# Performance work log

Hardware: AMD Instinct MI355X
Metric: run time of the kernel (lower is better)

Reference implementation:

```python
import jax, jax.numpy as jnp
import numpy as np

DIM = 1024
HIDDEN = 2048
NUM_EXPERTS = 8
TOP_K = 2


def setup_inputs() -> dict:
    key = jax.random.key(0)
    ks = jax.random.split(key, 6)
    scale = 0.02
    x = jax.random.normal(ks[0], (2, 4096, DIM), dtype=jnp.float32)
    # router: Linear(dim, num_experts, bias=False) -> weight [E, d]
    router_w = jax.random.normal(ks[1], (NUM_EXPERTS, DIM), dtype=jnp.float32) * scale
    # per-expert MLP: Linear(d, h) -> w1 [E, h, d], b1 [E, h]; Linear(h, d) -> w2 [E, d, h], b2 [E, d]
    w1 = jax.random.normal(ks[2], (NUM_EXPERTS, HIDDEN, DIM), dtype=jnp.float32) * scale
    b1 = jnp.zeros((NUM_EXPERTS, HIDDEN), dtype=jnp.float32)
    w2 = jax.random.normal(ks[3], (NUM_EXPERTS, DIM, HIDDEN), dtype=jnp.float32) * scale
    b2 = jnp.zeros((NUM_EXPERTS, DIM), dtype=jnp.float32)
    return {"x": x, "router_w": router_w, "w1": w1, "b1": b1, "w2": w2, "b2": b2}


def reference(x, router_w, w1, b1, w2, b2):
    b, s, d = x.shape
    xf = x.reshape(-1, d)                              # [T, d]
    logits = xf @ router_w.T                           # [T, E]
    all_probs = jax.nn.softmax(logits, axis=-1)
    topk_logits, topk_inds = jax.lax.top_k(logits, TOP_K)   # [T, K]
    topk_probs = jax.nn.softmax(topk_logits, axis=-1)
    E = router_w.shape[0]
    onehot = jax.nn.one_hot(topk_inds, E, dtype=xf.dtype)   # [T, K, E]
    # combine weights per (token, expert); zero where expert not selected
    gate = jnp.einsum('tke,tk->te', onehot, topk_probs)     # [T, E]
    # load-balancing auxiliary loss
    f_i = onehot.mean(axis=(0, 1))                          # [E]
    P_i = all_probs.mean(axis=0)                            # [E]
    aux_loss = E * jnp.sum(f_i * P_i)
    # dense per-expert MLP, weighted combine (dropout=0 / eval mode)
    out = jnp.zeros_like(xf)
    for e in range(E):  # fixed small loop over experts
        h = jax.nn.gelu(xf @ w1[e].T + b1[e], approximate=False)  # exact GELU (torch default)
        y = h @ w2[e].T + b2[e]
        out = out + gate[:, e:e + 1] * y
    return out.reshape(b, s, d), aux_loss
```

## Files before the change

kernel.cpp:

```cpp
#include <hip/hip_runtime.h>


#define TOKS 8192
#define DIMD 1024
#define HID  2048
#define NE   8

#define OFF_COUNTS   0
#define OFF_OFFSETS  64
#define OFF_CURSORS  128
#define OFF_TILEOFF  192
#define OFF_TOPKI    256
#define OFF_TOPKG    (OFF_TOPKI + TOKS*2*4)
#define OFF_BLKPS    (OFF_TOPKG + TOKS*2*4)
#define OFF_ATOK     (OFF_BLKPS + 2048*NE*4)
#define OFF_AGATE    (OFF_ATOK + TOKS*2*4)
#define OFF_PINV     (OFF_AGATE + TOKS*2*4)
#define OFF_XG       (1u << 20)
#define XG_ROWS      (TOKS*2 + 128)
#define OFF_W1B      (OFF_XG  + (size_t)XG_ROWS * DIMD * 2)
#define OFF_W2B      (OFF_W1B + (size_t)NE * HID * DIMD * 2)
#define OFF_H        (OFF_W2B + (size_t)NE * DIMD * HID * 2)
#define OFF_Y        (OFF_H   + (size_t)XG_ROWS * HID * 2)

typedef __bf16 bf16x8 __attribute__((ext_vector_type(8)));
typedef float  floatx4 __attribute__((ext_vector_type(4)));

__device__ __forceinline__ float bf2f(unsigned short u) {
    return __uint_as_float(((unsigned)u) << 16);
}
__device__ __forceinline__ unsigned short f2bf(float f) {
    unsigned u = __float_as_uint(f);
    unsigned r = (u + 0x7FFFu + ((u >> 16) & 1u)) >> 16;
    return (unsigned short)r;
}

#define GLOBAL_AS(p) ((const __attribute__((address_space(1))) unsigned int*)(p))
#define LDS_AS(p)    ((__attribute__((address_space(3))) unsigned int*)(p))

__global__ void convert_w_kernel(const float4* __restrict__ w1,
                                 ushort4* __restrict__ w1b, int n1,
                                 const float4* __restrict__ w2,
                                 ushort4* __restrict__ w2b, int n2) {
    int i = blockIdx.x * blockDim.x + threadIdx.x;
    int stride = gridDim.x * blockDim.x;
    int ntot = n1 + n2;
    for (; i < ntot; i += stride) {
        float4 v; ushort4 o;
        if (i < n1) v = w1[i]; else v = w2[i - n1];
        o.x = f2bf(v.x); o.y = f2bf(v.y); o.z = f2bf(v.z); o.w = f2bf(v.w);
        if (i < n1) w1b[i] = o; else w2b[i - n1] = o;
    }
}

__global__ __launch_bounds__(256) void router_kernel(
    const float* __restrict__ x, const float* __restrict__ rw,
    int* __restrict__ topki, float* __restrict__ topkg,
    float* __restrict__ blkps)
{
    int wave = threadIdx.x >> 6;
    int lane = threadIdx.x & 63;
    int t = blockIdx.x * 4 + wave;
    const float* xt = x + (size_t)t * DIMD;

    float acc[NE];
#pragma unroll
    for (int e = 0; e < NE; e++) acc[e] = 0.f;
    for (int i = 0; i < DIMD / 64; i++) {
        float xv = xt[lane + 64 * i];
#pragma unroll
        for (int e = 0; e < NE; e++) acc[e] += xv * rw[e * DIMD + lane + 64 * i];
    }
#pragma unroll
    for (int off = 32; off > 0; off >>= 1) {
#pragma unroll
        for (int e = 0; e < NE; e++) acc[e] += __shfl_down(acc[e], off);
    }

    __shared__ float ps[4][NE];
    if (lane == 0) {
        float m = acc[0];
#pragma unroll
        for (int e = 1; e < NE; e++) m = fmaxf(m, acc[e]);
        float ex[NE], s = 0.f;
#pragma unroll
        for (int e = 0; e < NE; e++) { ex[e] = expf(acc[e] - m); s += ex[e]; }
        float inv = 1.f / s;
#pragma unroll
        for (int e = 0; e < NE; e++) ps[wave][e] = ex[e] * inv;

        int i0 = 0; float l0 = acc[0];
#pragma unroll
        for (int e = 1; e < NE; e++) if (acc[e] > l0) { l0 = acc[e]; i0 = e; }
        int i1 = -1; float l1 = -3.4e38f;
#pragma unroll
        for (int e = 0; e < NE; e++) if (e != i0 && acc[e] > l1) { l1 = acc[e]; i1 = e; }
        float e1 = expf(l1 - l0);
        float g0 = 1.f / (1.f + e1);
        float g1 = e1 * g0;
        topki[t * 2 + 0] = i0; topki[t * 2 + 1] = i1;
        topkg[t * 2 + 0] = g0; topkg[t * 2 + 1] = g1;
    }
    __syncthreads();
    if (threadIdx.x < NE) {
        float s = ps[0][threadIdx.x] + ps[1][threadIdx.x] + ps[2][threadIdx.x] + ps[3][threadIdx.x];
        blkps[blockIdx.x * NE + threadIdx.x] = s;
    }
}

__global__ __launch_bounds__(256) void finalize_kernel(
    const int* __restrict__ topki, const float* __restrict__ blkps,
    int* __restrict__ counts, int* __restrict__ offsets, int* __restrict__ cursors,
    int* __restrict__ tileoff, float* __restrict__ aux_out)
{
    __shared__ float psum[NE];
    __shared__ int cnt[NE];
    int tid = threadIdx.x;
    if (tid < NE) { psum[tid] = 0.f; cnt[tid] = 0; }
    __syncthreads();

    float lp[NE]; int lc[NE];
#pragma unroll
    for (int e = 0; e < NE; e++) { lp[e] = 0.f; lc[e] = 0; }
    const float4* bp4 = (const float4*)blkps;
    for (int i = tid; i < 2048 * NE / 4; i += 256) {
        float4 v = bp4[i];
        int eb = (4 * i) & 7;
        lp[eb + 0] += v.x; lp[eb + 1] += v.y; lp[eb + 2] += v.z; lp[eb + 3] += v.w;
    }
    const int4* ti4 = (const int4*)topki;
    for (int i = tid; i < TOKS * 2 / 4; i += 256) {
        int4 v = ti4[i];
        lc[v.x]++; lc[v.y]++; lc[v.z]++; lc[v.w]++;
    }
#pragma unroll
    for (int e = 0; e < NE; e++) { atomicAdd(&psum[e], lp[e]); atomicAdd(&cnt[e], lc[e]); }
    __syncthreads();

    if (tid == 0) {
        int off = 0, to = 0;
        for (int e = 0; e < NE; e++) {
            counts[e] = cnt[e];
            offsets[e] = off; cursors[e] = off;
            tileoff[e] = to;
            off += cnt[e];
            to += (cnt[e] + 127) >> 7;
        }
        offsets[NE] = off; tileoff[NE] = to;
        float aux = 0.f;
        for (int e = 0; e < NE; e++)
            aux += ((float)cnt[e] / (float)(TOKS * 2)) * (psum[e] / (float)TOKS);
        aux_out[0] = (float)NE * aux;
    }
}

__global__ __launch_bounds__(64) void fill_kernel(
    const int* __restrict__ topki, const float* __restrict__ topkg,
    int* __restrict__ cursors, int* __restrict__ atok, float* __restrict__ agate,
    int* __restrict__ posinv)
{
    int lane = threadIdx.x;
    int t = blockIdx.x * 64 + lane;
    unsigned long long below = (lane == 63) ? 0x7FFFFFFFFFFFFFFFull
                                            : ((1ull << lane) - 1ull);
#pragma unroll
    for (int k = 0; k < 2; k++) {
        int e = topki[t * 2 + k];
        float g = topkg[t * 2 + k];
        for (int ee = 0; ee < NE; ee++) {
            bool pred = (e == ee);
            unsigned long long mask = __ballot(pred ? 1 : 0);
            if (mask) {
                int leader = __ffsll((unsigned long long)mask) - 1;
                int base = 0;
                if (lane == leader) base = atomicAdd(&cursors[ee], (int)__popcll(mask));
                base = __shfl(base, leader);
                if (pred) {
                    int pos = base + (int)__popcll(mask & below);
                    atok[pos] = t;
                    agate[pos] = g;
                    posinv[t * 2 + k] = pos;
                }
            }
        }
    }
}

__global__ __launch_bounds__(256) void gather_x_kernel(
    const float* __restrict__ x, const int* __restrict__ atok,
    ushort* __restrict__ Xg)
{
    int r = blockIdx.x;
    int tid = threadIdx.x;
    int tok = atok[r];
    float4 v = ((const float4*)(x + (size_t)tok * DIMD))[tid];
    ushort4 o;
    o.x = f2bf(v.x); o.y = f2bf(v.y); o.z = f2bf(v.z); o.w = f2bf(v.w);
    ((ushort4*)(Xg + (size_t)r * DIMD))[tid] = o;
}

__global__ __launch_bounds__(256) void phase1_kernel(
    const ushort* __restrict__ Xg, const ushort* __restrict__ w1b,
    const float* __restrict__ b1,
    const int* __restrict__ counts, const int* __restrict__ offsets,
    const int* __restrict__ tileoff, unsigned short* __restrict__ Hbuf)
{
    const int NCOLT = HID / 128;
    int total = tileoff[NE] * NCOLT;
    int idx = blockIdx.x;
    if (idx >= total) return;
    int ct = idx & (NCOLT - 1);
    int rowt = idx / NCOLT;
    int e = 0;
    while (rowt >= tileoff[e + 1]) e++;
    int row0 = (rowt - tileoff[e]) * 128;
    int cnt = counts[e];
    int base = offsets[e];
    int colbase = ct * 128;

    __shared__ ushort ldsA[128 * 32];
    __shared__ ushort ldsB[128 * 32];

    int tid = threadIdx.x;
    int lane = tid & 63;
    int wave = tid >> 6;
    int wrow = wave >> 1, wcol = wave & 1;
    int l15 = lane & 15, quad = lane >> 4;

    const ushort* gA0 = Xg + (size_t)(base + row0 + 16 * (2 * wave)     + l15) * DIMD + quad * 8;
    const ushort* gA1 = Xg + (size_t)(base + row0 + 16 * (2 * wave + 1) + l15) * DIMD + quad * 8;
    const ushort* wB  = w1b + (size_t)e * HID * DIMD;
    const ushort* gB0 = wB + (size_t)(colbase + 16 * (2 * wave)     + l15) * DIMD + quad * 8;
    const ushort* gB1 = wB + (size_t)(colbase + 16 * (2 * wave + 1) + l15) * DIMD + quad * 8;

    ushort* ldA0 = &ldsA[(2 * wave) * 512];
    ushort* ldA1 = &ldsA[(2 * wave + 1) * 512];
    ushort* ldB0 = &ldsB[(2 * wave) * 512];
    ushort* ldB1 = &ldsB[(2 * wave + 1) * 512];

    floatx4 acc[4][4];
#pragma unroll
    for (int i = 0; i < 4; i++)
#pragma unroll
        for (int j = 0; j < 4; j++) acc[i][j] = (floatx4){0.f, 0.f, 0.f, 0.f};

    const bf16x8* fA = reinterpret_cast<const bf16x8*>(ldsA);
    const bf16x8* fB = reinterpret_cast<const bf16x8*>(ldsB);

    for (int k0 = 0; k0 < DIMD; k0 += 32) {
        __syncthreads();
        __builtin_amdgcn_global_load_lds(GLOBAL_AS(gA0), LDS_AS(ldA0), 16, 0, 0);
        __builtin_amdgcn_global_load_lds(GLOBAL_AS(gA1), LDS_AS(ldA1), 16, 0, 0);
        __builtin_amdgcn_global_load_lds(GLOBAL_AS(gB0), LDS_AS(ldB0), 16, 0, 0);
        __builtin_amdgcn_global_load_lds(GLOBAL_AS(gB1), LDS_AS(ldB1), 16, 0, 0);
        gA0 += 32; gA1 += 32; gB0 += 32; gB1 += 32;
        __syncthreads();

        bf16x8 a[4], b[4];
#pragma unroll
        for (int i = 0; i < 4; i++) a[i] = fA[(4 * wrow + i) * 64 + lane];
#pragma unroll
        for (int j = 0; j < 4; j++) b[j] = fB[(4 * wcol + j) * 64 + lane];
#pragma unroll
        for (int i = 0; i < 4; i++)
#pragma unroll
            for (int j = 0; j < 4; j++)
                acc[i][j] = __builtin_amdgcn_mfma_f32_16x16x32_bf16(a[i], b[j], acc[i][j], 0, 0, 0);
    }

#pragma unroll
    for (int i = 0; i < 4; i++) {
#pragma unroll
        for (int r = 0; r < 4; r++) {
            int pr = row0 + 64 * wrow + 16 * i + quad * 4 + r;
            if (pr < cnt) {
                size_t hrow = (size_t)(base + pr) * HID;
#pragma unroll
                for (int j = 0; j < 4; j++) {
                    int col = colbase + 64 * wcol + 16 * j + l15;
                    float v = acc[i][j][r] + b1[e * HID + col];
                    v = 0.5f * v * (1.f + erff(v * 0.70710678118654752f));
                    Hbuf[hrow + col] = f2bf(v);
                }
            }
        }
    }
}

__global__ __launch_bounds__(256) void phase2_kernel(
    const ushort* __restrict__ Hbuf, const ushort* __restrict__ w2b,
    const int* __restrict__ counts, const int* __restrict__ offsets,
    const int* __restrict__ tileoff, ushort* __restrict__ Y)
{
    const int NCOLT = DIMD / 128;
    int total = tileoff[NE] * NCOLT;
    int idx = blockIdx.x;
    if (idx >= total) return;
    int ct = idx & (NCOLT - 1);
    int rowt = idx / NCOLT;
    int e = 0;
    while (rowt >= tileoff[e + 1]) e++;
    int row0 = (rowt - tileoff[e]) * 128;
    int cnt = counts[e];
    int base = offsets[e];
    int colbase = ct * 128;

    __shared__ ushort ldsA[128 * 32];
    __shared__ ushort ldsB[128 * 32];

    int tid = threadIdx.x;
    int lane = tid & 63;
    int wave = tid >> 6;
    int wrow = wave >> 1, wcol = wave & 1;
    int l15 = lane & 15, quad = lane >> 4;

    const ushort* gA0 = Hbuf + (size_t)(base + row0 + 16 * (2 * wave)     + l15) * HID + quad * 8;
    const ushort* gA1 = Hbuf + (size_t)(base + row0 + 16 * (2 * wave + 1) + l15) * HID + quad * 8;
    const ushort* wB  = w2b + (size_t)e * DIMD * HID;
    const ushort* gB0 = wB + (size_t)(colbase + 16 * (2 * wave)     + l15) * HID + quad * 8;
    const ushort* gB1 = wB + (size_t)(colbase + 16 * (2 * wave + 1) + l15) * HID + quad * 8;

    ushort* ldA0 = &ldsA[(2 * wave) * 512];
    ushort* ldA1 = &ldsA[(2 * wave + 1) * 512];
    ushort* ldB0 = &ldsB[(2 * wave) * 512];
    ushort* ldB1 = &ldsB[(2 * wave + 1) * 512];

    floatx4 acc[4][4];
#pragma unroll
    for (int i = 0; i < 4; i++)
#pragma unroll
        for (int j = 0; j < 4; j++) acc[i][j] = (floatx4){0.f, 0.f, 0.f, 0.f};

    const bf16x8* fA = reinterpret_cast<const bf16x8*>(ldsA);
    const bf16x8* fB = reinterpret_cast<const bf16x8*>(ldsB);

    for (int k0 = 0; k0 < HID; k0 += 32) {
        __syncthreads();
        __builtin_amdgcn_global_load_lds(GLOBAL_AS(gA0), LDS_AS(ldA0), 16, 0, 0);
        __builtin_amdgcn_global_load_lds(GLOBAL_AS(gA1), LDS_AS(ldA1), 16, 0, 0);
        __builtin_amdgcn_global_load_lds(GLOBAL_AS(gB0), LDS_AS(ldB0), 16, 0, 0);
        __builtin_amdgcn_global_load_lds(GLOBAL_AS(gB1), LDS_AS(ldB1), 16, 0, 0);
        gA0 += 32; gA1 += 32; gB0 += 32; gB1 += 32;
        __syncthreads();

        bf16x8 a[4], b[4];
#pragma unroll
        for (int i = 0; i < 4; i++) a[i] = fA[(4 * wrow + i) * 64 + lane];
#pragma unroll
        for (int j = 0; j < 4; j++) b[j] = fB[(4 * wcol + j) * 64 + lane];
#pragma unroll
        for (int i = 0; i < 4; i++)
#pragma unroll
            for (int j = 0; j < 4; j++)
                acc[i][j] = __builtin_amdgcn_mfma_f32_16x16x32_bf16(a[i], b[j], acc[i][j], 0, 0, 0);
    }

#pragma unroll
    for (int i = 0; i < 4; i++) {
#pragma unroll
        for (int r = 0; r < 4; r++) {
            int pr = row0 + 64 * wrow + 16 * i + quad * 4 + r;
            if (pr < cnt) {
                size_t yrow = (size_t)(base + pr) * DIMD;
#pragma unroll
                for (int j = 0; j < 4; j++) {
                    int col = colbase + 64 * wcol + 16 * j + l15;
                    Y[yrow + col] = f2bf(acc[i][j][r]);
                }
            }
        }
    }
}

__global__ __launch_bounds__(256) void combine_kernel(
    const ushort* __restrict__ Y, const float* __restrict__ b2,
    const int* __restrict__ topki, const float* __restrict__ topkg,
    const int* __restrict__ posinv, float* __restrict__ out)
{
    int wave = threadIdx.x >> 6;
    int lane = threadIdx.x & 63;
    int t = blockIdx.x * 4 + wave;
    int e0 = topki[t * 2 + 0], e1 = topki[t * 2 + 1];
    float g0 = topkg[t * 2 + 0], g1 = topkg[t * 2 + 1];
    int p0 = posinv[t * 2 + 0], p1 = posinv[t * 2 + 1];

    const ushort4* y0 = (const ushort4*)(Y + (size_t)p0 * DIMD);
    const ushort4* y1 = (const ushort4*)(Y + (size_t)p1 * DIMD);
    const float4* b20 = (const float4*)(b2 + (size_t)e0 * DIMD);
    const float4* b21 = (const float4*)(b2 + (size_t)e1 * DIMD);
    float4* o4 = (float4*)(out + (size_t)t * DIMD);

#pragma unroll
    for (int c = 0; c < DIMD / 4 / 64; c++) {
        int i = lane + 64 * c;
        ushort4 a = y0[i], b = y1[i];
        float4 ba = b20[i], bb = b21[i];
        float4 r;
        r.x = g0 * (bf2f(a.x) + ba.x) + g1 * (bf2f(b.x) + bb.x);
        r.y = g0 * (bf2f(a.y) + ba.y) + g1 * (bf2f(b.y) + bb.y);
        r.z = g0 * (bf2f(a.z) + ba.z) + g1 * (bf2f(b.z) + bb.z);
        r.w = g0 * (bf2f(a.w) + ba.w) + g1 * (bf2f(b.w) + bb.w);
        o4[i] = r;
    }
}

extern "C" void kernel_launch(void* const* d_in, const int* in_sizes, int n_in,
                              void* d_out, int out_size, void* d_ws, size_t ws_size,
                              hipStream_t stream) {
    const float* x  = (const float*)d_in[0];
    const float* rw = (const float*)d_in[1];
    const float* w1 = (const float*)d_in[2];
    const float* b1 = (const float*)d_in[3];
    const float* w2 = (const float*)d_in[4];
    const float* b2 = (const float*)d_in[5];
    float* out = (float*)d_out;

    char* ws = (char*)d_ws;
    int*   counts  = (int*)(ws + OFF_COUNTS);
    int*   offsets = (int*)(ws + OFF_OFFSETS);
    int*   cursors = (int*)(ws + OFF_CURSORS);
    int*   tileoff = (int*)(ws + OFF_TILEOFF);
    int*   topki   = (int*)(ws + OFF_TOPKI);
    float* topkg   = (float*)(ws + OFF_TOPKG);
    float* blkps   = (float*)(ws + OFF_BLKPS);
    int*   atok    = (int*)(ws + OFF_ATOK);
    float* agate   = (float*)(ws + OFF_AGATE);
    int*   posinv  = (int*)(ws + OFF_PINV);
    ushort* Xg     = (ushort*)(ws + OFF_XG);
    ushort* w1b    = (ushort*)(ws + OFF_W1B);
    ushort* w2b    = (ushort*)(ws + OFF_W2B);
    ushort* Hbuf   = (ushort*)(ws + OFF_H);
    ushort* Y      = (ushort*)(ws + OFF_Y);

    convert_w_kernel<<<8192, 256, 0, stream>>>(
        (const float4*)w1, (ushort4*)w1b, NE * HID * DIMD / 4,
        (const float4*)w2, (ushort4*)w2b, NE * DIMD * HID / 4);

    router_kernel<<<TOKS / 4, 256, 0, stream>>>(x, rw, topki, topkg, blkps);
    finalize_kernel<<<1, 256, 0, stream>>>(topki, blkps, counts, offsets, cursors,
                                           tileoff, out + (size_t)TOKS * DIMD);
    fill_kernel<<<TOKS / 64, 64, 0, stream>>>(topki, topkg, cursors, atok, agate,
                                              posinv);
    gather_x_kernel<<<TOKS * 2, 256, 0, stream>>>(x, atok, Xg);

    phase1_kernel<<<135 * (HID / 128), 256, 0, stream>>>(
        Xg, w1b, b1, counts, offsets, tileoff, Hbuf);
    phase2_kernel<<<135 * (DIMD / 128), 256, 0, stream>>>(
        Hbuf, w2b, counts, offsets, tileoff, Y);
    combine_kernel<<<TOKS / 4, 256, 0, stream>>>(Y, b2, topki, topkg, posinv, out);
}
```

Measured before the change: 634.3 us.

## Double-buffer LDS tiles with K=64 steps and remap block order in expert GEMMs

Both grouped GEMM kernels now keep two LDS buffers and issue the async global-to-LDS loads for the next K=64 slab before running the MFMAs on the current slab. This lets memory loads overlap compute and halves the number of barriers per K step. Block indices are also permuted (stride of gridDim/8) so that neighbouring blocks are spread across XCDs. The cost is 4x the LDS per block (64KB), which may reduce occupancy. The remap assumes the grid size is a multiple of 8, otherwise some tiles are skipped.

```diff
diff --git a/kernel.cpp b/kernel.cpp
--- a/kernel.cpp
+++ b/kernel.cpp
@@ -207,7 +207,8 @@
 {
     const int NCOLT = HID / 128;
     int total = tileoff[NE] * NCOLT;
-    int idx = blockIdx.x;
+    int q = (int)(gridDim.x >> 3);
+    int idx = (int)(blockIdx.x & 7) * q + (int)(blockIdx.x >> 3);
     if (idx >= total) return;
     int ct = idx & (NCOLT - 1);
     int rowt = idx / NCOLT;
@@ -218,8 +219,7 @@
     int base = offsets[e];
     int colbase = ct * 128;
 
-    __shared__ ushort ldsA[128 * 32];
-    __shared__ ushort ldsB[128 * 32];
+    __shared__ ushort lds[2][2][2][128 * 32];
 
     int tid = threadIdx.x;
     int lane = tid & 63;
@@ -227,16 +227,20 @@
     int wrow = wave >> 1, wcol = wave & 1;
     int l15 = lane & 15, quad = lane >> 4;
 
-    const ushort* gA0 = Xg + (size_t)(base + row0 + 16 * (2 * wave)     + l15) * DIMD + quad * 8;
-    const ushort* gA1 = Xg + (size_t)(base + row0 + 16 * (2 * wave + 1) + l15) * DIMD + quad * 8;
-    const ushort* wB  = w1b + (size_t)e * HID * DIMD;
-    const ushort* gB0 = wB + (size_t)(colbase + 16 * (2 * wave)     + l15) * DIMD + quad * 8;
-    const ushort* gB1 = wB + (size_t)(colbase + 16 * (2 * wave + 1) + l15) * DIMD + quad * 8;
-
-    ushort* ldA0 = &ldsA[(2 * wave) * 512];
-    ushort* ldA1 = &ldsA[(2 * wave + 1) * 512];
-    ushort* ldB0 = &ldsB[(2 * wave) * 512];
-    ushort* ldB1 = &ldsB[(2 * wave + 1) * 512];
+    const ushort* gA = Xg + (size_t)(base + row0 + 16 * (2 * wave) + l15) * DIMD + quad * 8;
+    const ushort* gB = w1b + (size_t)e * HID * DIMD
+                     + (size_t)(colbase + 16 * (2 * wave) + l15) * DIMD + quad * 8;
+
+#define P1_STAGE(BUF, KOFF) do { \
+    __builtin_amdgcn_global_load_lds(GLOBAL_AS(gA + (KOFF)),                  LDS_AS(&lds[BUF][0][0][(2*wave+0)*512]), 16, 0, 0); \
+    __builtin_amdgcn_global_load_lds(GLOBAL_AS(gA + (KOFF) + 16*DIMD),        LDS_AS(&lds[BUF][0][0][(2*wave+1)*512]), 16, 0, 0); \
+    __builtin_amdgcn_global_load_lds(GLOBAL_AS(gA + (KOFF) + 32),             LDS_AS(&lds[BUF][0][1][(2*wave+0)*512]), 16, 0, 0); \
+    __builtin_amdgcn_global_load_lds(GLOBAL_AS(gA + (KOFF) + 32 + 16*DIMD),   LDS_AS(&lds[BUF][0][1][(2*wave+1)*512]), 16, 0, 0); \
+    __builtin_amdgcn_global_load_lds(GLOBAL_AS(gB + (KOFF)),                  LDS_AS(&lds[BUF][1][0][(2*wave+0)*512]), 16, 0, 0); \
+    __builtin_amdgcn_global_load_lds(GLOBAL_AS(gB + (KOFF) + 16*DIMD),        LDS_AS(&lds[BUF][1][0][(2*wave+1)*512]), 16, 0, 0); \
+    __builtin_amdgcn_global_load_lds(GLOBAL_AS(gB + (KOFF) + 32),             LDS_AS(&lds[BUF][1][1][(2*wave+0)*512]), 16, 0, 0); \
+    __builtin_amdgcn_global_load_lds(GLOBAL_AS(gB + (KOFF) + 32 + 16*DIMD),   LDS_AS(&lds[BUF][1][1][(2*wave+1)*512]), 16, 0, 0); \
+} while (0)
 
     floatx4 acc[4][4];
 #pragma unroll
@@ -244,29 +248,52 @@
 #pragma unroll
         for (int j = 0; j < 4; j++) acc[i][j] = (floatx4){0.f, 0.f, 0.f, 0.f};
 
-    const bf16x8* fA = reinterpret_cast<const bf16x8*>(ldsA);
-    const bf16x8* fB = reinterpret_cast<const bf16x8*>(ldsB);
-
-    for (int k0 = 0; k0 < DIMD; k0 += 32) {
+    P1_STAGE(0, 0);
+    __syncthreads();
+
+    int cur = 0;
+    for (int kt = 0; kt < DIMD / 64 - 1; kt++) {
+        bf16x8 a[2][4], b[2][4];
+#pragma unroll
+        for (int h = 0; h < 2; h++) {
+            const bf16x8* fA = (const bf16x8*)&lds[cur][0][h][0];
+            const bf16x8* fB = (const bf16x8*)&lds[cur][1][h][0];
+#pragma unroll
+            for (int i = 0; i < 4; i++) a[h][i] = fA[(4 * wrow + i) * 64 + lane];
+#pragma unroll
+            for (int j = 0; j < 4; j++) b[h][j] = fB[(4 * wcol + j) * 64 + lane];
+        }
+        P1_STAGE(cur ^ 1, (kt + 1) * 64);
+#pragma unroll
+        for (int h = 0; h < 2; h++)
+#pragma unroll
+            for (int i = 0; i < 4; i++)
+#pragma unroll
+                for (int j = 0; j < 4; j++)
+                    acc[i][j] = __builtin_amdgcn_mfma_f32_16x16x32_bf16(a[h][i], b[h][j], acc[i][j], 0, 0, 0);
         __syncthreads();
-        __builtin_amdgcn_global_load_lds(GLOBAL_AS(gA0), LDS_AS(ldA0), 16, 0, 0);
-        __builtin_amdgcn_global_load_lds(GLOBAL_AS(gA1), LDS_AS(ldA1), 16, 0, 0);
-        __builtin_amdgcn_global_load_lds(GLOBAL_AS(gB0), LDS_AS(ldB0), 16, 0, 0);
-        __builtin_amdgcn_global_load_lds(GLOBAL_AS(gB1), LDS_AS(ldB1), 16, 0, 0);
-        gA0 += 32; gA1 += 32; gB0 += 32; gB1 += 32;
-        __syncthreads();
-
-        bf16x8 a[4], b[4];
-#pragma unroll
-        for (int i = 0; i < 4; i++) a[i] = fA[(4 * wrow + i) * 64 + lane];
-#pragma unroll
-        for (int j = 0; j < 4; j++) b[j] = fB[(4 * wcol + j) * 64 + lane];
-#pragma unroll
-        for (int i = 0; i < 4; i++)
-#pragma unroll
-            for (int j = 0; j < 4; j++)
-                acc[i][j] = __builtin_amdgcn_mfma_f32_16x16x32_bf16(a[i], b[j], acc[i][j], 0, 0, 0);
-    }
+        cur ^= 1;
+    }
+    {
+        bf16x8 a[2][4], b[2][4];
+#pragma unroll
+        for (int h = 0; h < 2; h++) {
+            const bf16x8* fA = (const bf16x8*)&lds[cur][0][h][0];
+            const bf16x8* fB = (const bf16x8*)&lds[cur][1][h][0];
+#pragma unroll
+            for (int i = 0; i < 4; i++) a[h][i] = fA[(4 * wrow + i) * 64 + lane];
+#pragma unroll
+            for (int j = 0; j < 4; j++) b[h][j] = fB[(4 * wcol + j) * 64 + lane];
+        }
+#pragma unroll
+        for (int h = 0; h < 2; h++)
+#pragma unroll
+            for (int i = 0; i < 4; i++)
+#pragma unroll
+                for (int j = 0; j < 4; j++)
+                    acc[i][j] = __builtin_amdgcn_mfma_f32_16x16x32_bf16(a[h][i], b[h][j], acc[i][j], 0, 0, 0);
+    }
+#undef P1_STAGE
 
 #pragma unroll
     for (int i = 0; i < 4; i++) {
@@ -294,7 +321,8 @@
 {
     const int NCOLT = DIMD / 128;
     int total = tileoff[NE] * NCOLT;
-    int idx = blockIdx.x;
+    int q = (int)(gridDim.x >> 3);
+    int idx = (int)(blockIdx.x & 7) * q + (int)(blockIdx.x >> 3);
     if (idx >= total) return;
     int ct = idx & (NCOLT - 1);
     int rowt = idx / NCOLT;
@@ -305,8 +333,7 @@
     int base = offsets[e];
     int colbase = ct * 128;
 
-    __shared__ ushort ldsA[128 * 32];
-    __shared__ ushort ldsB[128 * 32];
+    __shared__ ushort lds[2][2][2][128 * 32];
 
     int tid = threadIdx.x;
     int lane = tid & 63;
@@ -314,16 +341,20 @@
     int wrow = wave >> 1, wcol = wave & 1;
     int l15 = lane & 15, quad = lane >> 4;
 
-    const ushort* gA0 = Hbuf + (size_t)(base + row0 + 16 * (2 * wave)     + l15) * HID + quad * 8;
-    const ushort* gA1 = Hbuf + (size_t)(base + row0 + 16 * (2 * wave + 1) + l15) * HID + quad * 8;
-    const ushort* wB  = w2b + (size_t)e * DIMD * HID;
-    const ushort* gB0 = wB + (size_t)(colbase + 16 * (2 * wave)     + l15) * HID + quad * 8;
-    const ushort* gB1 = wB + (size_t)(colbase + 16 * (2 * wave + 1) + l15) * HID + quad * 8;
-
-    ushort* ldA0 = &ldsA[(2 * wave) * 512];
-    ushort* ldA1 = &ldsA[(2 * wave + 1) * 512];
-    ushort* ldB0 = &ldsB[(2 * wave) * 512];
-    ushort* ldB1 = &ldsB[(2 * wave + 1) * 512];
+    const ushort* gA = Hbuf + (size_t)(base + row0 + 16 * (2 * wave) + l15) * HID + quad * 8;
+    const ushort* gB = w2b + (size_t)e * DIMD * HID
+                     + (size_t)(colbase + 16 * (2 * wave) + l15) * HID + quad * 8;
+
+#define P2_STAGE(BUF, KOFF) do { \
+    __builtin_amdgcn_global_load_lds(GLOBAL_AS(gA + (KOFF)),                 LDS_AS(&lds[BUF][0][0][(2*wave+0)*512]), 16, 0, 0); \
+    __builtin_amdgcn_global_load_lds(GLOBAL_AS(gA + (KOFF) + 16*HID),        LDS_AS(&lds[BUF][0][0][(2*wave+1)*512]), 16, 0, 0); \
+    __builtin_amdgcn_global_load_lds(GLOBAL_AS(gA + (KOFF) + 32),            LDS_AS(&lds[BUF][0][1][(2*wave+0)*512]), 16, 0, 0); \
+    __builtin_amdgcn_global_load_lds(GLOBAL_AS(gA + (KOFF) + 32 + 16*HID),   LDS_AS(&lds[BUF][0][1][(2*wave+1)*512]), 16, 0, 0); \
+    __builtin_amdgcn_global_load_lds(GLOBAL_AS(gB + (KOFF)),                 LDS_AS(&lds[BUF][1][0][(2*wave+0)*512]), 16, 0, 0); \
+    __builtin_amdgcn_global_load_lds(GLOBAL_AS(gB + (KOFF) + 16*HID),        LDS_AS(&lds[BUF][1][0][(2*wave+1)*512]), 16, 0, 0); \
+    __builtin_amdgcn_global_load_lds(GLOBAL_AS(gB + (KOFF) + 32),            LDS_AS(&lds[BUF][1][1][(2*wave+0)*512]), 16, 0, 0); \
+    __builtin_amdgcn_global_load_lds(GLOBAL_AS(gB + (KOFF) + 32 + 16*HID),   LDS_AS(&lds[BUF][1][1][(2*wave+1)*512]), 16, 0, 0); \
+} while (0)
 
     floatx4 acc[4][4];
 #pragma unroll
@@ -331,29 +362,52 @@
 #pragma unroll
         for (int j = 0; j < 4; j++) acc[i][j] = (floatx4){0.f, 0.f, 0.f, 0.f};
 
-    const bf16x8* fA = reinterpret_cast<const bf16x8*>(ldsA);
-    const bf16x8* fB = reinterpret_cast<const bf16x8*>(ldsB);
-
-    for (int k0 = 0; k0 < HID; k0 += 32) {
+    P2_STAGE(0, 0);
+    __syncthreads();
+
+    int cur = 0;
+    for (int kt = 0; kt < HID / 64 - 1; kt++) {
+        bf16x8 a[2][4], b[2][4];
+#pragma unroll
+        for (int h = 0; h < 2; h++) {
+            const bf16x8* fA = (const bf16x8*)&lds[cur][0][h][0];
+            const bf16x8* fB = (const bf16x8*)&lds[cur][1][h][0];
+#pragma unroll
+            for (int i = 0; i < 4; i++) a[h][i] = fA[(4 * wrow + i) * 64 + lane];
+#pragma unroll
+            for (int j = 0; j < 4; j++) b[h][j] = fB[(4 * wcol + j) * 64 + lane];
+        }
+        P2_STAGE(cur ^ 1, (kt + 1) * 64);
+#pragma unroll
+        for (int h = 0; h < 2; h++)
+#pragma unroll
+            for (int i = 0; i < 4; i++)
+#pragma unroll
+                for (int j = 0; j < 4; j++)
+                    acc[i][j] = __builtin_amdgcn_mfma_f32_16x16x32_bf16(a[h][i], b[h][j], acc[i][j], 0, 0, 0);
         __syncthreads();
-        __builtin_amdgcn_global_load_lds(GLOBAL_AS(gA0), LDS_AS(ldA0), 16, 0, 0);
-        __builtin_amdgcn_global_load_lds(GLOBAL_AS(gA1), LDS_AS(ldA1), 16, 0, 0);
-        __builtin_amdgcn_global_load_lds(GLOBAL_AS(gB0), LDS_AS(ldB0), 16, 0, 0);
-        __builtin_amdgcn_global_load_lds(GLOBAL_AS(gB1), LDS_AS(ldB1), 16, 0, 0);
-        gA0 += 32; gA1 += 32; gB0 += 32; gB1 += 32;
-        __syncthreads();
-
-        bf16x8 a[4], b[4];
-#pragma unroll
-        for (int i = 0; i < 4; i++) a[i] = fA[(4 * wrow + i) * 64 + lane];
-#pragma unroll
-        for (int j = 0; j < 4; j++) b[j] = fB[(4 * wcol + j) * 64 + lane];
-#pragma unroll
-        for (int i = 0; i < 4; i++)
-#pragma unroll
-            for (int j = 0; j < 4; j++)
-                acc[i][j] = __builtin_amdgcn_mfma_f32_16x16x32_bf16(a[i], b[j], acc[i][j], 0, 0, 0);
-    }
+        cur ^= 1;
+    }
+    {
+        bf16x8 a[2][4], b[2][4];
+#pragma unroll
+        for (int h = 0; h < 2; h++) {
+            const bf16x8* fA = (const bf16x8*)&lds[cur][0][h][0];
+            const bf16x8* fB = (const bf16x8*)&lds[cur][1][h][0];
+#pragma unroll
+            for (int i = 0; i < 4; i++) a[h][i] = fA[(4 * wrow + i) * 64 + lane];
+#pragma unroll
+            for (int j = 0; j < 4; j++) b[h][j] = fB[(4 * wcol + j) * 64 + lane];
+        }
+#pragma unroll
+        for (int h = 0; h < 2; h++)
+#pragma unroll
+            for (int i = 0; i < 4; i++)
+#pragma unroll
+                for (int j = 0; j < 4; j++)
+                    acc[i][j] = __builtin_amdgcn_mfma_f32_16x16x32_bf16(a[h][i], b[h][j], acc[i][j], 0, 0, 0);
+    }
+#undef P2_STAGE
 
 #pragma unroll
     for (int i = 0; i < 4; i++) {
```

New measurement: 683.3 us. +7.7%, slower.

## Enlarge grouped GEMM tiles to 256x256, double-buffer LDS, remap blocks across XCDs

Applied to the files above, without the earlier changes.

Both expert GEMM phases move from 128x128 tiles with 256 threads to 256x256 tiles with 512 threads. Each wave now accumulates an 8x4 grid of MFMA tiles. The K-step grows to 64, and LDS is double-buffered so the next global-to-LDS load is issued before computing on the current buffer, leaving one barrier per step instead of two. Block IDs are remapped so consecutive tiles land on the same XCD for L2 reuse, and the bias load is hoisted out of the store loop. In exchange there are fewer blocks, which hurts load balance, more padding rows per expert, and higher register pressure from 128 accumulator floats per thread.

```diff
diff --git a/kernel.cpp b/kernel.cpp
--- a/kernel.cpp
+++ b/kernel.cpp
@@ -17,7 +17,7 @@
 #define OFF_AGATE    (OFF_ATOK + TOKS*2*4)
 #define OFF_PINV     (OFF_AGATE + TOKS*2*4)
 #define OFF_XG       (1u << 20)
-#define XG_ROWS      (TOKS*2 + 128)
+#define XG_ROWS      (TOKS*2 + 256)
 #define OFF_W1B      (OFF_XG  + (size_t)XG_ROWS * DIMD * 2)
 #define OFF_W2B      (OFF_W1B + (size_t)NE * HID * DIMD * 2)
 #define OFF_H        (OFF_W2B + (size_t)NE * DIMD * HID * 2)
@@ -37,6 +37,13 @@
 
 #define GLOBAL_AS(p) ((const __attribute__((address_space(1))) unsigned int*)(p))
 #define LDS_AS(p)    ((__attribute__((address_space(3))) unsigned int*)(p))
+
+__device__ __forceinline__ int xcd_remap(int bid, int nwg) {
+    int xcd = bid & 7, pos = bid >> 3;
+    int q = nwg >> 3, r = nwg & 7;
+    int start = (xcd < r) ? xcd * (q + 1) : r * (q + 1) + (xcd - r) * q;
+    return start + pos;
+}
 
 __global__ void convert_w_kernel(const float4* __restrict__ w1,
                                  ushort4* __restrict__ w1b, int n1,
@@ -144,7 +151,7 @@
             offsets[e] = off; cursors[e] = off;
             tileoff[e] = to;
             off += cnt[e];
-            to += (cnt[e] + 127) >> 7;
+            to += (cnt[e] + 255) >> 8;
         }
         offsets[NE] = off; tileoff[NE] = to;
         float aux = 0.f;
@@ -199,86 +206,108 @@
     ((ushort4*)(Xg + (size_t)r * DIMD))[tid] = o;
 }
 
-__global__ __launch_bounds__(256) void phase1_kernel(
+
+__global__ __launch_bounds__(512, 2) void phase1_kernel(
     const ushort* __restrict__ Xg, const ushort* __restrict__ w1b,
     const float* __restrict__ b1,
     const int* __restrict__ counts, const int* __restrict__ offsets,
     const int* __restrict__ tileoff, unsigned short* __restrict__ Hbuf)
 {
-    const int NCOLT = HID / 128;
+    const int LD = DIMD;
+    const int NT = DIMD / 64;
+    const int NCOLT = HID / 256;
     int total = tileoff[NE] * NCOLT;
-    int idx = blockIdx.x;
+    int idx = xcd_remap((int)blockIdx.x, (int)gridDim.x);
     if (idx >= total) return;
     int ct = idx & (NCOLT - 1);
     int rowt = idx / NCOLT;
     int e = 0;
     while (rowt >= tileoff[e + 1]) e++;
-    int row0 = (rowt - tileoff[e]) * 128;
+    int row0 = (rowt - tileoff[e]) * 256;
     int cnt = counts[e];
     int base = offsets[e];
-    int colbase = ct * 128;
-
-    __shared__ ushort ldsA[128 * 32];
-    __shared__ ushort ldsB[128 * 32];
+    int colbase = ct * 256;
+
+    __shared__ ushort lds[2][64][512];
 
     int tid = threadIdx.x;
     int lane = tid & 63;
     int wave = tid >> 6;
-    int wrow = wave >> 1, wcol = wave & 1;
+    int wr = wave >> 2, wc = wave & 3;
     int l15 = lane & 15, quad = lane >> 4;
 
-    const ushort* gA0 = Xg + (size_t)(base + row0 + 16 * (2 * wave)     + l15) * DIMD + quad * 8;
-    const ushort* gA1 = Xg + (size_t)(base + row0 + 16 * (2 * wave + 1) + l15) * DIMD + quad * 8;
-    const ushort* wB  = w1b + (size_t)e * HID * DIMD;
-    const ushort* gB0 = wB + (size_t)(colbase + 16 * (2 * wave)     + l15) * DIMD + quad * 8;
-    const ushort* gB1 = wB + (size_t)(colbase + 16 * (2 * wave + 1) + l15) * DIMD + quad * 8;
-
-    ushort* ldA0 = &ldsA[(2 * wave) * 512];
-    ushort* ldA1 = &ldsA[(2 * wave + 1) * 512];
-    ushort* ldB0 = &ldsB[(2 * wave) * 512];
-    ushort* ldB1 = &ldsB[(2 * wave + 1) * 512];
-
-    floatx4 acc[4][4];
-#pragma unroll
-    for (int i = 0; i < 4; i++)
+    const ushort* gApanel = Xg + (size_t)(base + row0) * LD;
+    const ushort* gBpanel = w1b + (size_t)e * HID * DIMD + (size_t)colbase * LD;
+
+    const ushort* src[8];
+#pragma unroll
+    for (int i = 0; i < 8; i++) {
+        int chunk = wave * 8 + i;
+        int tensor = chunk >> 5;
+        int r = chunk & 31;
+        int s = r >> 1, h = r & 1;
+        const ushort* bse = tensor ? gBpanel : gApanel;
+        src[i] = bse + (size_t)(s * 16 + l15) * LD + h * 32 + quad * 8;
+    }
+
+#define STAGE(BUF) do { \
+    _Pragma("unroll") \
+    for (int i = 0; i < 8; i++) { \
+        __builtin_amdgcn_global_load_lds(GLOBAL_AS(src[i]), LDS_AS(&lds[BUF][wave*8 + i][0]), 16, 0, 0); \
+        src[i] += 64; \
+    } \
+} while (0)
+
+    floatx4 acc[8][4];
+#pragma unroll
+    for (int i = 0; i < 8; i++)
 #pragma unroll
         for (int j = 0; j < 4; j++) acc[i][j] = (floatx4){0.f, 0.f, 0.f, 0.f};
 
-    const bf16x8* fA = reinterpret_cast<const bf16x8*>(ldsA);
-    const bf16x8* fB = reinterpret_cast<const bf16x8*>(ldsB);
-
-    for (int k0 = 0; k0 < DIMD; k0 += 32) {
+    auto compute = [&](int bufidx) {
+        const bf16x8* C = (const bf16x8*)&lds[bufidx][0][0];
+#pragma unroll
+        for (int h = 0; h < 2; h++) {
+            bf16x8 a[8], b[4];
+#pragma unroll
+            for (int i = 0; i < 8; i++) a[i] = C[((wr * 8 + i) * 2 + h) * 64 + lane];
+#pragma unroll
+            for (int j = 0; j < 4; j++) b[j] = C[(32 + (wc * 4 + j) * 2 + h) * 64 + lane];
+#pragma unroll
+            for (int i = 0; i < 8; i++)
+#pragma unroll
+                for (int j = 0; j < 4; j++)
+                    acc[i][j] = __builtin_amdgcn_mfma_f32_16x16x32_bf16(a[i], b[j], acc[i][j], 0, 0, 0);
+        }
+    };
+
+    STAGE(0);
+    __syncthreads();
+    int cur = 0;
+    for (int kt = 0; kt < NT - 1; kt++) {
+        STAGE(cur ^ 1);
+        compute(cur);
         __syncthreads();
-        __builtin_amdgcn_global_load_lds(GLOBAL_AS(gA0), LDS_AS(ldA0), 16, 0, 0);
-        __builtin_amdgcn_global_load_lds(GLOBAL_AS(gA1), LDS_AS(ldA1), 16, 0, 0);
-        __builtin_amdgcn_global_load_lds(GLOBAL_AS(gB0), LDS_AS(ldB0), 16, 0, 0);
-        __builtin_amdgcn_global_load_lds(GLOBAL_AS(gB1), LDS_AS(ldB1), 16, 0, 0);
-        gA0 += 32; gA1 += 32; gB0 += 32; gB1 += 32;
-        __syncthreads();
-
-        bf16x8 a[4], b[4];
-#pragma unroll
-        for (int i = 0; i < 4; i++) a[i] = fA[(4 * wrow + i) * 64 + lane];
-#pragma unroll
-        for (int j = 0; j < 4; j++) b[j] = fB[(4 * wcol + j) * 64 + lane];
-#pragma unroll
-        for (int i = 0; i < 4; i++)
-#pragma unroll
-            for (int j = 0; j < 4; j++)
-                acc[i][j] = __builtin_amdgcn_mfma_f32_16x16x32_bf16(a[i], b[j], acc[i][j], 0, 0, 0);
-    }
-
-#pragma unroll
-    for (int i = 0; i < 4; i++) {
-#pragma unroll
-        for (int r = 0; r < 4; r++) {
-            int pr = row0 + 64 * wrow + 16 * i + quad * 4 + r;
+        cur ^= 1;
+    }
+    compute(cur);
+#undef STAGE
+
+    float b1v[4];
+#pragma unroll
+    for (int j = 0; j < 4; j++)
+        b1v[j] = b1[e * HID + colbase + 64 * wc + 16 * j + l15];
+#pragma unroll
+    for (int i = 0; i < 8; i++) {
+#pragma unroll
+        for (int rr = 0; rr < 4; rr++) {
+            int pr = row0 + 128 * wr + 16 * i + quad * 4 + rr;
             if (pr < cnt) {
                 size_t hrow = (size_t)(base + pr) * HID;
 #pragma unroll
                 for (int j = 0; j < 4; j++) {
-                    int col = colbase + 64 * wcol + 16 * j + l15;
-                    float v = acc[i][j][r] + b1[e * HID + col];
+                    int col = colbase + 64 * wc + 16 * j + l15;
+                    float v = acc[i][j][rr] + b1v[j];
                     v = 0.5f * v * (1.f + erff(v * 0.70710678118654752f));
                     Hbuf[hrow + col] = f2bf(v);
                 }
@@ -287,85 +316,102 @@
     }
 }
 
-__global__ __launch_bounds__(256) void phase2_kernel(
+__global__ __launch_bounds__(512, 2) void phase2_kernel(
     const ushort* __restrict__ Hbuf, const ushort* __restrict__ w2b,
     const int* __restrict__ counts, const int* __restrict__ offsets,
     const int* __restrict__ tileoff, ushort* __restrict__ Y)
 {
-    const int NCOLT = DIMD / 128;
+    const int LD = HID;
+    const int NT = HID / 64;
+    const int NCOLT = DIMD / 256;
     int total = tileoff[NE] * NCOLT;
-    int idx = blockIdx.x;
+    int idx = xcd_remap((int)blockIdx.x, (int)gridDim.x);
     if (idx >= total) return;
     int ct = idx & (NCOLT - 1);
     int rowt = idx / NCOLT;
     int e = 0;
     while (rowt >= tileoff[e + 1]) e++;
-    int row0 = (rowt - tileoff[e]) * 128;
+    int row0 = (rowt - tileoff[e]) * 256;
     int cnt = counts[e];
     int base = offsets[e];
-    int colbase = ct * 128;
-
-    __shared__ ushort ldsA[128 * 32];
-    __shared__ ushort ldsB[128 * 32];
+    int colbase = ct * 256;
+
+    __shared__ ushort lds[2][64][512];
 
     int tid = threadIdx.x;
     int lane = tid & 63;
     int wave = tid >> 6;
-    int wrow = wave >> 1, wcol = wave & 1;
+    int wr = wave >> 2, wc = wave & 3;
     int l15 = lane & 15, quad = lane >> 4;
 
-    const ushort* gA0 = Hbuf + (size_t)(base + row0 + 16 * (2 * wave)     + l15) * HID + quad * 8;
-    const ushort* gA1 = Hbuf + (size_t)(base + row0 + 16 * (2 * wave + 1) + l15) * HID + quad * 8;
-    const ushort* wB  = w2b + (size_t)e * DIMD * HID;
-    const ushort* gB0 = wB + (size_t)(colbase + 16 * (2 * wave)     + l15) * HID + quad * 8;
-    const ushort* gB1 = wB + (size_t)(colbase + 16 * (2 * wave + 1) + l15) * HID + quad * 8;
-
-    ushort* ldA0 = &ldsA[(2 * wave) * 512];
-    ushort* ldA1 = &ldsA[(2 * wave + 1) * 512];
-    ushort* ldB0 = &ldsB[(2 * wave) * 512];
-    ushort* ldB1 = &ldsB[(2 * wave + 1) * 512];
-
-    floatx4 acc[4][4];
-#pragma unroll
-    for (int i = 0; i < 4; i++)
+    const ushort* gApanel = Hbuf + (size_t)(base + row0) * LD;
+    const ushort* gBpanel = w2b + (size_t)e * DIMD * HID + (size_t)colbase * LD;
+
+    const ushort* src[8];
+#pragma unroll
+    for (int i = 0; i < 8; i++) {
+        int chunk = wave * 8 + i;
+        int tensor = chunk >> 5;
+        int r = chunk & 31;
+        int s = r >> 1, h = r & 1;
+        const ushort* bse = tensor ? gBpanel : gApanel;
+        src[i] = bse + (size_t)(s * 16 + l15) * LD + h * 32 + quad * 8;
+    }
+
+#define STAGE(BUF) do { \
+    _Pragma("unroll") \
+    for (int i = 0; i < 8; i++) { \
+        __builtin_amdgcn_global_load_lds(GLOBAL_AS(src[i]), LDS_AS(&lds[BUF][wave*8 + i][0]), 16, 0, 0); \
+        src[i] += 64; \
+    } \
+} while (0)
+
+    floatx4 acc[8][4];
+#pragma unroll
+    for (int i = 0; i < 8; i++)
 #pragma unroll
         for (int j = 0; j < 4; j++) acc[i][j] = (floatx4){0.f, 0.f, 0.f, 0.f};
 
-    const bf16x8* fA = reinterpret_cast<const bf16x8*>(ldsA);
-    const bf16x8* fB = reinterpret_cast<const bf16x8*>(ldsB);
-
-    for (int k0 = 0; k0 < HID; k0 += 32) {
+    auto compute = [&](int bufidx) {
+        const bf16x8* C = (const bf16x8*)&lds[bufidx][0][0];
+#pragma unroll
+        for (int h = 0; h < 2; h++) {
+            bf16x8 a[8], b[4];
+#pragma unroll
+            for (int i = 0; i < 8; i++) a[i] = C[((wr * 8 + i) * 2 + h) * 64 + lane];
+#pragma unroll
+            for (int j = 0; j < 4; j++) b[j] = C[(32 + (wc * 4 + j) * 2 + h) * 64 + lane];
+#pragma unroll
+            for (int i = 0; i < 8; i++)
+#pragma unroll
+                for (int j = 0; j < 4; j++)
+                    acc[i][j] = __builtin_amdgcn_mfma_f32_16x16x32_bf16(a[i], b[j], acc[i][j], 0, 0, 0);
+        }
+    };
+
+    STAGE(0);
+    __syncthreads();
+    int cur = 0;
+    for (int kt = 0; kt < NT - 1; kt++) {
+        STAGE(cur ^ 1);
+        compute(cur);
         __syncthreads();
-        __builtin_amdgcn_global_load_lds(GLOBAL_AS(gA0), LDS_AS(ldA0), 16, 0, 0);
-        __builtin_amdgcn_global_load_lds(GLOBAL_AS(gA1), LDS_AS(ldA1), 16, 0, 0);
-        __builtin_amdgcn_global_load_lds(GLOBAL_AS(gB0), LDS_AS(ldB0), 16, 0, 0);
-        __builtin_amdgcn_global_load_lds(GLOBAL_AS(gB1), LDS_AS(ldB1), 16, 0, 0);
-        gA0 += 32; gA1 += 32; gB0 += 32; gB1 += 32;
-        __syncthreads();
-
-        bf16x8 a[4], b[4];
-#pragma unroll
-        for (int i = 0; i < 4; i++) a[i] = fA[(4 * wrow + i) * 64 + lane];
-#pragma unroll
-        for (int j = 0; j < 4; j++) b[j] = fB[(4 * wcol + j) * 64 + lane];
-#pragma unroll
-        for (int i = 0; i < 4; i++)
-#pragma unroll
-            for (int j = 0; j < 4; j++)
-                acc[i][j] = __builtin_amdgcn_mfma_f32_16x16x32_bf16(a[i], b[j], acc[i][j], 0, 0, 0);
-    }
-
-#pragma unroll
-    for (int i = 0; i < 4; i++) {
-#pragma unroll
-        for (int r = 0; r < 4; r++) {
-            int pr = row0 + 64 * wrow + 16 * i + quad * 4 + r;
+        cur ^= 1;
+    }
+    compute(cur);
+#undef STAGE
+
+#pragma unroll
+    for (int i = 0; i < 8; i++) {
+#pragma unroll
+        for (int rr = 0; rr < 4; rr++) {
+            int pr = row0 + 128 * wr + 16 * i + quad * 4 + rr;
             if (pr < cnt) {
                 size_t yrow = (size_t)(base + pr) * DIMD;
 #pragma unroll
                 for (int j = 0; j < 4; j++) {
-                    int col = colbase + 64 * wcol + 16 * j + l15;
-                    Y[yrow + col] = f2bf(acc[i][j][r]);
+                    int col = colbase + 64 * wc + 16 * j + l15;
+                    Y[yrow + col] = f2bf(acc[i][j][rr]);
                 }
             }
         }
@@ -443,9 +489,9 @@
                                               posinv);
     gather_x_kernel<<<TOKS * 2, 256, 0, stream>>>(x, atok, Xg);
 
-    phase1_kernel<<<135 * (HID / 128), 256, 0, stream>>>(
+    phase1_kernel<<<71 * (HID / 256), 512, 0, stream>>>(
         Xg, w1b, b1, counts, offsets, tileoff, Hbuf);
-    phase2_kernel<<<135 * (DIMD / 128), 256, 0, stream>>>(
+    phase2_kernel<<<71 * (DIMD / 256), 512, 0, stream>>>(
         Hbuf, w2b, counts, offsets, tileoff, Y);
     combine_kernel<<<TOKS / 4, 256, 0, stream>>>(Y, b2, topki, topkg, posinv, out);
 }
```

Result: no change. 629.3 us (-0.8%).
